# Kernel tuning notes

Hardware: AMD Instinct MI355X
Metric: run time of the kernel (lower is better)

Reference implementation:

```python
import jax, jax.numpy as jnp
import numpy as np

N5, N4, N3, K = 10242, 2562, 642, 7  # icosphere node counts (levels 5,4,3), spatial kernel size
M = 32  # mchannel
EPS = 1e-8


def _sconv(x, neigh, W, b, relu=True):
    # x: [B,T,N,Cin]; neigh: [N,K] 1-ring indices; W: [K,Cin,Cout]
    xn = x[:, :, neigh, :]                        # [B,T,N,K,Cin] irregular gather
    y = jnp.einsum('btnkc,kcd->btnd', xn, W) + b  # per-node kernel contraction
    return jax.nn.relu(y) if relu else y


def _spool(x, pidx):
    # max-pool fine->coarse mesh: pidx [Ncoarse,Kp] indexes fine nodes
    return jnp.max(x[:, :, pidx, :], axis=3)


def _unpool(x, uidx):
    # coarse->fine copy: uidx [Nfine] indexes coarse nodes
    return x[:, :, uidx, :]


def _cos(f, a):
    # torch.nn.CosineSimilarity(dim=-1): dot / max(|f|*|a|, eps)
    dot = jnp.sum(f * a, axis=-1)
    nf = jnp.linalg.norm(f, axis=-1)
    na = jnp.linalg.norm(a, axis=-1)
    return dot / jnp.maximum(nf * na, EPS)


def setup_inputs() -> dict:
    key = jax.random.key(0)
    ks = jax.random.split(key, 32)
    w = lambda i, shape: jax.random.normal(ks[i], shape, jnp.float32) * 0.05
    inp = {
        'frame': jax.random.normal(ks[0], (1, 16, N5, 3), jnp.float32),
        'aem': jax.random.normal(ks[1], (1, 16, N5), jnp.float32),
        'W0f': w(2, (K, 3, M)),        'b0f': w(3, (M,)),
        'W0a': w(4, (K, 1, M)),        'b0a': w(5, (M,)),
        'W1f': w(6, (K, M, 2 * M)),    'b1f': w(7, (2 * M,)),
        'W1a': w(8, (K, M, 2 * M)),    'b1a': w(9, (2 * M,)),
        'W2f': w(10, (K, 2 * M, 4 * M)), 'b2f': w(11, (4 * M,)),
        'W2a': w(12, (K, 2 * M, 4 * M)), 'b2a': w(13, (4 * M,)),
        'W7': w(14, (K, 12 * M, 2 * M)), 'b7': w(15, (2 * M,)),
        'W8': w(16, (K, 4 * M, M)),    'b8': w(17, (M,)),
        'W9': w(18, (K, M, 1)),        'b9': w(19, (1,)),
        'neigh5': jax.random.randint(ks[20], (N5, K), 0, N5),
        'neigh4': jax.random.randint(ks[21], (N4, K), 0, N4),
        'neigh3': jax.random.randint(ks[22], (N3, K), 0, N3),
        'pool5': jax.random.randint(ks[23], (N4, K), 0, N5),
        'pool4': jax.random.randint(ks[24], (N3, K), 0, N4),
        'up4': jax.random.randint(ks[25], (N4,), 0, N3),
        'up5': jax.random.randint(ks[26], (N5,), 0, N4),
        'Tlocation': jax.random.randint(ks[27], (1, 16), 0, 16),
    }
    return inp


def reference(frame, aem, W0f, b0f, W0a, b0a, W1f, b1f, W1a, b1a, W2f, b2f,
              W2a, b2a, W7, b7, W8, b8, W9, b9,
              neigh5, neigh4, neigh3, pool5, pool4, up4, up5, Tlocation):
    a = aem[..., None]                                    # [B,T,N5,1]
    # encoder level 0 (N5)
    c0f = _sconv(frame, neigh5, W0f, b0f)
    c0a = _sconv(a, neigh5, W0a, b0a)
    p0f = _spool(c0f, pool5)
    p0a = _spool(c0a, pool5)
    m0 = _cos(c0f, c0a)[..., None]                        # [B,T,N5,1]
    c0f_att, c0a_att = c0f * m0, c0a * m0
    # encoder level 1 (N4)
    c1f = _sconv(p0f, neigh4, W1f, b1f)
    c1a = _sconv(p0a, neigh4, W1a, b1a)
    p1f = _spool(c1f, pool4)
    p1a = _spool(c1a, pool4)
    m1 = _cos(c1f, c1a)[..., None]
    c1f_att, c1a_att = c1f * m1, c1a * m1
    # bottleneck (N3)
    c2f = _sconv(p1f, neigh3, W2f, b2f)
    c2a = _sconv(p1a, neigh3, W2a, b2a)
    m2 = _cos(c2f, c2a)[..., None]
    conv2 = jnp.concatenate((c2f * m2, c2a * m2), axis=-1)  # [B,T,N3,8M]
    # decoder
    cat7 = jnp.concatenate((_unpool(conv2, up4), c1f_att, c1a_att), axis=-1)  # [B,T,N4,12M]
    conv7 = _sconv(cat7, neigh4, W7, b7)
    cat8 = jnp.concatenate((_unpool(conv7, up5), c0f_att, c0a_att), axis=-1)  # [B,T,N5,4M]
    conv8 = _sconv(cat8, neigh5, W8, b8)
    conv9 = _sconv(conv8, neigh5, W9, b9, relu=False)[..., 0]  # [B,T,N5]
    return jax.nn.softmax(conv9, axis=-1)
```

## Files before the change

kernel.cpp:

```cpp
#include <hip/hip_runtime.h>
#include <cfloat>
#include <cstdint>


constexpr int T  = 16;
constexpr int n5 = 10242, n4 = 2562, n3 = 642;
constexpr int K  = 7;

using bf16x8 = __attribute__((ext_vector_type(8))) short;
using f32x4  = __attribute__((ext_vector_type(4))) float;

static __device__ __forceinline__ float bf2f(unsigned short u) {
    return __uint_as_float((unsigned)u << 16);
}
static __device__ __forceinline__ unsigned short f2bf(float x) {
    unsigned u = __float_as_uint(x);
    u += 0x7FFF + ((u >> 16) & 1);
    return (unsigned short)(u >> 16);
}

__global__ __launch_bounds__(256) void conv0_kernel(
    const float* __restrict__ frame, const float* __restrict__ aem,
    const float* __restrict__ W0f, const float* __restrict__ b0f,
    const float* __restrict__ W0a, const float* __restrict__ b0a,
    const int* __restrict__ neigh5,
    unsigned short* __restrict__ c0f, unsigned short* __restrict__ c0a,
    unsigned short* __restrict__ att0)
{
    const int g = threadIdx.x >> 5;
    const int d = threadIdx.x & 31;
    const int per_t = (n5 + 7) / 8;
    const int t = blockIdx.x / per_t;
    const int n = (blockIdx.x % per_t) * 8 + g;
    if (n >= n5) return;

    float accf = b0f[d];
    float acca = b0a[d];
    const int* nb = neigh5 + n * K;
    #pragma unroll
    for (int k = 0; k < K; ++k) {
        const int j = nb[k];
        const float* fr = frame + ((size_t)t * n5 + j) * 3;
        const float av = aem[(size_t)t * n5 + j];
        accf = fmaf(fr[0], W0f[(k * 3 + 0) * 32 + d], accf);
        accf = fmaf(fr[1], W0f[(k * 3 + 1) * 32 + d], accf);
        accf = fmaf(fr[2], W0f[(k * 3 + 2) * 32 + d], accf);
        acca = fmaf(av, W0a[k * 32 + d], acca);
    }
    accf = fmaxf(accf, 0.f);
    acca = fmaxf(acca, 0.f);

    float dot = accf * acca, ff = accf * accf, aa = acca * acca;
    #pragma unroll
    for (int m = 1; m < 32; m <<= 1) {
        dot += __shfl_xor(dot, m, 32);
        ff  += __shfl_xor(ff,  m, 32);
        aa  += __shfl_xor(aa,  m, 32);
    }
    const float mm = dot / fmaxf(sqrtf(ff) * sqrtf(aa), 1e-8f);
    const size_t base = ((size_t)t * n5 + n) * 32;
    c0f[base + d] = f2bf(accf);
    c0a[base + d] = f2bf(acca);
    const size_t abase = ((size_t)t * n5 + n) * 64;
    att0[abase + d]      = f2bf(accf * mm);
    att0[abase + 32 + d] = f2bf(acca * mm);
}

template<int C>
__global__ __launch_bounds__(256) void pool_kernel(
    const unsigned short* __restrict__ in, const int* __restrict__ pidx,
    int Nin, int Nout, unsigned short* __restrict__ out)
{
    constexpr int C8 = C / 8;
    const int idx = blockIdx.x * 256 + threadIdx.x;
    if (idx >= T * Nout * C8) return;
    const int c8 = idx % C8;
    const int n  = (idx / C8) % Nout;
    const int t  = idx / (C8 * Nout);
    const int* pp = pidx + n * K;
    float m[8];
    #pragma unroll
    for (int j = 0; j < 8; ++j) m[j] = -FLT_MAX;
    #pragma unroll
    for (int k = 0; k < K; ++k) {
        const uint4 v = reinterpret_cast<const uint4*>(in)[((size_t)t * Nin + pp[k]) * C8 + c8];
        const unsigned short* s = reinterpret_cast<const unsigned short*>(&v);
        #pragma unroll
        for (int j = 0; j < 8; ++j) m[j] = fmaxf(m[j], bf2f(s[j]));
    }
    unsigned short o[8];
    #pragma unroll
    for (int j = 0; j < 8; ++j) o[j] = f2bf(m[j]);
    reinterpret_cast<uint4*>(out)[((size_t)t * Nout + n) * C8 + c8] =
        *reinterpret_cast<const uint4*>(o);
}

template<int C, int NN>
__global__ __launch_bounds__(256) void cosatt_kernel(
    const unsigned short* __restrict__ f, const unsigned short* __restrict__ a,
    unsigned short* __restrict__ att)
{
    constexpr int CPL = C / 64;
    const int w = threadIdx.x >> 6, lane = threadIdx.x & 63;
    const int idx = blockIdx.x * 4 + w;
    if (idx >= T * NN) return;
    const unsigned short* fr = f + (size_t)idx * C;
    const unsigned short* ar = a + (size_t)idx * C;
    float xs[CPL], ys[CPL];
    float dot = 0.f, ff = 0.f, aa = 0.f;
    #pragma unroll
    for (int i = 0; i < CPL; ++i) {
        const float x = bf2f(fr[lane + i * 64]);
        const float y = bf2f(ar[lane + i * 64]);
        xs[i] = x; ys[i] = y;
        dot = fmaf(x, y, dot);
        ff  = fmaf(x, x, ff);
        aa  = fmaf(y, y, aa);
    }
    #pragma unroll
    for (int msk = 1; msk < 64; msk <<= 1) {
        dot += __shfl_xor(dot, msk);
        ff  += __shfl_xor(ff,  msk);
        aa  += __shfl_xor(aa,  msk);
    }
    const float m = dot / fmaxf(sqrtf(ff) * sqrtf(aa), 1e-8f);
    unsigned short* orow = att + (size_t)idx * 2 * C;
    #pragma unroll
    for (int i = 0; i < CPL; ++i) {
        orow[lane + i * 64]     = f2bf(xs[i] * m);
        orow[C + lane + i * 64] = f2bf(ys[i] * m);
    }
}

struct PlainB16 {
    const uint4* x; int N; int C8;
    struct Ref { int o; };
    __device__ __forceinline__ Ref prep(int t, int node) const {
        return { (int)(((size_t)t * N + node) * C8) };
    }
    __device__ __forceinline__ uint4 chunk(const Ref& r, int c8) const {
        return x[r.o + c8];
    }
};

struct Cat7B16 {
    const uint4* att2; const uint4* att1; const int* up4;
    struct Ref { int o2, o1; };
    __device__ __forceinline__ Ref prep(int t, int node) const {
        return { (int)(((size_t)t * n3 + up4[node]) * 32),
                 (int)(((size_t)t * n4 + node) * 16) };
    }
    __device__ __forceinline__ uint4 chunk(const Ref& r, int c8) const {
        return (c8 < 32) ? att2[r.o2 + c8] : att1[r.o1 + (c8 - 32)];
    }
};

struct Cat8B16 {
    const uint4* cv7; const uint4* att0; const int* up5;
    struct Ref { int o7, o0; };
    __device__ __forceinline__ Ref prep(int t, int node) const {
        return { (int)(((size_t)t * n4 + up5[node]) * 8),
                 (int)(((size_t)t * n5 + node) * 8) };
    }
    __device__ __forceinline__ uint4 chunk(const Ref& r, int c8) const {
        return (c8 < 8) ? cv7[r.o7 + c8] : att0[r.o0 + (c8 - 8)];
    }
};

__global__ __launch_bounds__(256) void wprep_all_kernel(
    const float* __restrict__ W1f, const float* __restrict__ W1a,
    const float* __restrict__ W2f, const float* __restrict__ W2a,
    const float* __restrict__ W7,  const float* __restrict__ W8,
    unsigned short* __restrict__ Wt1f, unsigned short* __restrict__ Wt1a,
    unsigned short* __restrict__ Wt2f, unsigned short* __restrict__ Wt2a,
    unsigned short* __restrict__ Wt7,  unsigned short* __restrict__ Wt8)
{
    int idx = blockIdx.x * 256 + threadIdx.x;
    const float* W; unsigned short* Wt; int KCv, CO;
    if (idx < 14336)       { W = W1f; Wt = Wt1f; KCv = 224;  CO = 64;  }
    else if (idx < 28672)  { idx -= 14336;  W = W1a; Wt = Wt1a; KCv = 224;  CO = 64;  }
    else if (idx < 86016)  { idx -= 28672;  W = W2f; Wt = Wt2f; KCv = 448;  CO = 128; }
    else if (idx < 143360) { idx -= 86016;  W = W2a; Wt = Wt2a; KCv = 448;  CO = 128; }
    else if (idx < 315392) { idx -= 143360; W = W7;  Wt = Wt7;  KCv = 2688; CO = 64;  }
    else                   { idx -= 315392; W = W8;  Wt = Wt8;  KCv = 896;  CO = 32;  }
    const int d = idx / KCv, kc = idx - d * KCv;
    Wt[idx] = f2bf(W[(size_t)kc * CO + d]);
}

template<int CIN, int COUT, class Loader>
__device__ __forceinline__ void sconv_tile(
    const Loader& ldr, const int* __restrict__ neigh, int N, int t,
    int tile_m, int tile_n,
    const unsigned short* __restrict__ Wt, const float* __restrict__ bias,
    unsigned short* __restrict__ out)
{
    constexpr int KC     = K * CIN;
    constexpr int CHUNKS = CIN / 32;
    constexpr int STEPS  = K * CHUNKS;
    constexpr int D      = STEPS < 3 ? STEPS : 3;

    const int lane = threadIdx.x & 63;
    const int l15 = lane & 15, lhi = lane >> 4;

    const int r0 = tile_m * 32 + l15;
    const int row0 = min(r0, N - 1), row1 = min(r0 + 16, N - 1);

    typename Loader::Ref ref0[K], ref1[K];
    #pragma unroll
    for (int k = 0; k < K; ++k) {
        ref0[k] = ldr.prep(t, neigh[row0 * K + k]);
        ref1[k] = ldr.prep(t, neigh[row1 * K + k]);
    }

    const int col0 = tile_n * 32 + l15;
    const unsigned short* w0p = Wt + (size_t)col0 * KC + lhi * 8;
    const unsigned short* w1p = w0p + (size_t)16 * KC;

    uint4 qa0[D], qa1[D], qb0[D], qb1[D];

    auto issue = [&](int s, int slot) {
        const int k = s / CHUNKS, c = s - k * CHUNKS;
        const int c8 = c * 4 + lhi;
        qa0[slot] = ldr.chunk(ref0[k], c8);
        qa1[slot] = ldr.chunk(ref1[k], c8);
        qb0[slot] = *reinterpret_cast<const uint4*>(w0p + k * CIN + c * 32);
        qb1[slot] = *reinterpret_cast<const uint4*>(w1p + k * CIN + c * 32);
    };

    f32x4 acc[2][2] = {};

    #pragma unroll
    for (int s = 0; s < D; ++s) issue(s, s);
    __builtin_amdgcn_sched_barrier(0);

    #pragma unroll
    for (int s = 0; s < STEPS; ++s) {
        const int slot = s % D;
        const bf16x8 a0 = __builtin_bit_cast(bf16x8, qa0[slot]);
        const bf16x8 a1 = __builtin_bit_cast(bf16x8, qa1[slot]);
        const bf16x8 b0 = __builtin_bit_cast(bf16x8, qb0[slot]);
        const bf16x8 b1 = __builtin_bit_cast(bf16x8, qb1[slot]);
        acc[0][0] = __builtin_amdgcn_mfma_f32_16x16x32_bf16(a0, b0, acc[0][0], 0, 0, 0);
        acc[0][1] = __builtin_amdgcn_mfma_f32_16x16x32_bf16(a0, b1, acc[0][1], 0, 0, 0);
        acc[1][0] = __builtin_amdgcn_mfma_f32_16x16x32_bf16(a1, b0, acc[1][0], 0, 0, 0);
        acc[1][1] = __builtin_amdgcn_mfma_f32_16x16x32_bf16(a1, b1, acc[1][1], 0, 0, 0);
        if (s + D < STEPS) issue(s + D, slot);
        __builtin_amdgcn_sched_barrier(0);
    }

    #pragma unroll
    for (int n = 0; n < 2; ++n) {
        const int gcol = tile_n * 32 + n * 16 + l15;
        const float bv = bias[gcol];
        #pragma unroll
        for (int m = 0; m < 2; ++m) {
            #pragma unroll
            for (int i = 0; i < 4; ++i) {
                const int grow = tile_m * 32 + m * 16 + lhi * 4 + i;
                if (grow < N)
                    out[((size_t)t * N + grow) * COUT + gcol] =
                        f2bf(fmaxf(acc[m][n][i] + bv, 0.f));
            }
        }
    }
}

template<int CIN, int COUT, class Loader>
__global__ __launch_bounds__(64, 2) void sconv_rd_kernel(
    Loader ldr, const int* __restrict__ neigh, int N, int U,
    const unsigned short* __restrict__ Wt, const float* __restrict__ bias,
    unsigned short* __restrict__ out)
{
    constexpr int TN = COUT / 32;
    const int xcd = blockIdx.x & 7;
    int idx = blockIdx.x >> 3;
    const int hi = (idx >= U) ? 1 : 0;
    const int t  = 2 * xcd + hi;
    const int w  = idx - hi * U;
    sconv_tile<CIN, COUT, Loader>(ldr, neigh, N, t, w / TN, w % TN, Wt, bias, out);
}

template<int CIN, int COUT, class Loader>
__global__ __launch_bounds__(64, 2) void sconv_rd2_kernel(
    Loader lf, Loader la, const int* __restrict__ neigh, int N, int U,
    const unsigned short* __restrict__ Wtf, const unsigned short* __restrict__ Wta,
    const float* __restrict__ bf_, const float* __restrict__ ba_,
    unsigned short* __restrict__ of_, unsigned short* __restrict__ oa_)
{
    constexpr int TN = COUT / 32;
    const int xcd = blockIdx.x & 7;
    int idx = blockIdx.x >> 3;
    const int sel = idx & 1; idx >>= 1;
    const int hi = (idx >= U) ? 1 : 0;
    const int t  = 2 * xcd + hi;
    const int w  = idx - hi * U;
    const Loader L = sel ? la : lf;
    const unsigned short* Wt = sel ? Wta : Wtf;
    const float* bias = sel ? ba_ : bf_;
    unsigned short* out = sel ? oa_ : of_;
    sconv_tile<CIN, COUT, Loader>(L, neigh, N, t, w / TN, w % TN, Wt, bias, out);
}

__global__ __launch_bounds__(256) void conv9_kernel(
    const unsigned short* __restrict__ cv8, const int* __restrict__ neigh5,
    const float* __restrict__ W9, const float* __restrict__ b9,
    float* __restrict__ logits)
{
    const int idx = blockIdx.x * 256 + threadIdx.x;
    if (idx >= T * n5) return;
    const int n = idx % n5;
    const int t = idx / n5;
    float acc = b9[0];
    const int* nb = neigh5 + n * K;
    #pragma unroll
    for (int k = 0; k < K; ++k) {
        const uint4* row = reinterpret_cast<const uint4*>(cv8 + ((size_t)t * n5 + nb[k]) * 32);
        const float* wk = W9 + k * 32;
        #pragma unroll
        for (int c4 = 0; c4 < 4; ++c4) {
            const uint4 v = row[c4];
            const unsigned short* s = reinterpret_cast<const unsigned short*>(&v);
            #pragma unroll
            for (int jj = 0; jj < 8; ++jj)
                acc = fmaf(bf2f(s[jj]), wk[c4 * 8 + jj], acc);
        }
    }
    logits[idx] = acc;
}

__global__ __launch_bounds__(1024) void softmax_kernel(
    const float* __restrict__ logits, float* __restrict__ out)
{
    const int t = blockIdx.x, tid = threadIdx.x;
    const float* x = logits + (size_t)t * n5;
    float* y = out + (size_t)t * n5;
    __shared__ float redmax[16], redsum[16];

    float mx = -FLT_MAX;
    for (int i = tid; i < n5; i += 1024) mx = fmaxf(mx, x[i]);
    #pragma unroll
    for (int m = 1; m < 64; m <<= 1) mx = fmaxf(mx, __shfl_xor(mx, m));
    if ((tid & 63) == 0) redmax[tid >> 6] = mx;
    __syncthreads();
    mx = redmax[0];
    #pragma unroll
    for (int i = 1; i < 16; ++i) mx = fmaxf(mx, redmax[i]);

    float s = 0.f;
    for (int i = tid; i < n5; i += 1024) s += expf(x[i] - mx);
    #pragma unroll
    for (int m = 1; m < 64; m <<= 1) s += __shfl_xor(s, m);
    if ((tid & 63) == 0) redsum[tid >> 6] = s;
    __syncthreads();
    s = 0.f;
    #pragma unroll
    for (int i = 0; i < 16; ++i) s += redsum[i];

    for (int i = tid; i < n5; i += 1024) y[i] = expf(x[i] - mx) / s;
}

extern "C" void kernel_launch(void* const* d_in, const int* in_sizes, int n_in,
                              void* d_out, int out_size, void* d_ws, size_t ws_size,
                              hipStream_t stream)
{
    const float* frame = (const float*)d_in[0];
    const float* aem   = (const float*)d_in[1];
    const float* W0f = (const float*)d_in[2];
    const float* b0f = (const float*)d_in[3];
    const float* W0a = (const float*)d_in[4];
    const float* b0a = (const float*)d_in[5];
    const float* W1f = (const float*)d_in[6];
    const float* b1f = (const float*)d_in[7];
    const float* W1a = (const float*)d_in[8];
    const float* b1a = (const float*)d_in[9];
    const float* W2f = (const float*)d_in[10];
    const float* b2f = (const float*)d_in[11];
    const float* W2a = (const float*)d_in[12];
    const float* b2a = (const float*)d_in[13];
    const float* W7  = (const float*)d_in[14];
    const float* b7  = (const float*)d_in[15];
    const float* W8  = (const float*)d_in[16];
    const float* b8  = (const float*)d_in[17];
    const float* W9  = (const float*)d_in[18];
    const float* b9  = (const float*)d_in[19];
    const int* neigh5 = (const int*)d_in[20];
    const int* neigh4 = (const int*)d_in[21];
    const int* neigh3 = (const int*)d_in[22];
    const int* pool5  = (const int*)d_in[23];
    const int* pool4  = (const int*)d_in[24];
    const int* up4    = (const int*)d_in[25];
    const int* up5    = (const int*)d_in[26];

    unsigned short* wsu = (unsigned short*)d_ws;
    size_t off = 0;
    auto ua = [&](size_t n) {
        unsigned short* p = wsu + off; off += (n + 7) & ~(size_t)7; return p;
    };
    unsigned short* c0f  = ua((size_t)T * n5 * 32);
    unsigned short* c0a  = ua((size_t)T * n5 * 32);
    unsigned short* att0 = ua((size_t)T * n5 * 64);
    unsigned short* p0f  = ua((size_t)T * n4 * 32);
    unsigned short* p0a  = ua((size_t)T * n4 * 32);
    unsigned short* c1f  = ua((size_t)T * n4 * 64);
    unsigned short* c1a  = ua((size_t)T * n4 * 64);
    unsigned short* att1 = ua((size_t)T * n4 * 128);
    unsigned short* p1f  = ua((size_t)T * n3 * 64);
    unsigned short* p1a  = ua((size_t)T * n3 * 64);
    unsigned short* c2f  = ua((size_t)T * n3 * 128);
    unsigned short* c2a  = ua((size_t)T * n3 * 128);
    unsigned short* att2 = ua((size_t)T * n3 * 256);
    unsigned short* cv7  = ua((size_t)T * n4 * 64);
    unsigned short* cv8  = ua((size_t)T * n5 * 32);
    unsigned short* Wt1f = ua((size_t)64 * 224);
    unsigned short* Wt1a = ua((size_t)64 * 224);
    unsigned short* Wt2f = ua((size_t)128 * 448);
    unsigned short* Wt2a = ua((size_t)128 * 448);
    unsigned short* Wt7  = ua((size_t)64 * 2688);
    unsigned short* Wt8  = ua((size_t)32 * 896);
    float* lgt = (float*)(wsu + off);

    wprep_all_kernel<<<1344, 256, 0, stream>>>(
        W1f, W1a, W2f, W2a, W7, W8, Wt1f, Wt1a, Wt2f, Wt2a, Wt7, Wt8);

    conv0_kernel<<<T * ((n5 + 7) / 8), 256, 0, stream>>>(
        frame, aem, W0f, b0f, W0a, b0a, neigh5, c0f, c0a, att0);

    {
        const int thr = T * n4 * (32 / 8);
        pool_kernel<32><<<(thr + 255) / 256, 256, 0, stream>>>(c0f, pool5, n5, n4, p0f);
        pool_kernel<32><<<(thr + 255) / 256, 256, 0, stream>>>(c0a, pool5, n5, n4, p0a);
    }

    {
        constexpr int U = 81 * 2;
        sconv_rd2_kernel<32, 64><<<8 * 4 * U, 64, 0, stream>>>(
            PlainB16{(const uint4*)p0f, n4, 4}, PlainB16{(const uint4*)p0a, n4, 4},
            neigh4, n4, U, Wt1f, Wt1a, b1f, b1a, c1f, c1a);
    }
    cosatt_kernel<64, n4><<<(T * n4 + 3) / 4, 256, 0, stream>>>(c1f, c1a, att1);

    {
        const int thr = T * n3 * (64 / 8);
        pool_kernel<64><<<(thr + 255) / 256, 256, 0, stream>>>(c1f, pool4, n4, n3, p1f);
        pool_kernel<64><<<(thr + 255) / 256, 256, 0, stream>>>(c1a, pool4, n4, n3, p1a);
    }

    {
        constexpr int U = 21 * 4;
        sconv_rd2_kernel<64, 128><<<8 * 4 * U, 64, 0, stream>>>(
            PlainB16{(const uint4*)p1f, n3, 8}, PlainB16{(const uint4*)p1a, n3, 8},
            neigh3, n3, U, Wt2f, Wt2a, b2f, b2a, c2f, c2a);
    }
    cosatt_kernel<128, n3><<<(T * n3 + 3) / 4, 256, 0, stream>>>(c2f, c2a, att2);

    {
        constexpr int U = 81 * 2;
        sconv_rd_kernel<384, 64><<<8 * 2 * U, 64, 0, stream>>>(
            Cat7B16{(const uint4*)att2, (const uint4*)att1, up4},
            neigh4, n4, U, Wt7, b7, cv7);
    }

    {
        constexpr int U = 321;
        sconv_rd_kernel<128, 32><<<8 * 2 * U, 64, 0, stream>>>(
            Cat8B16{(const uint4*)cv7, (const uint4*)att0, up5},
            neigh5, n5, U, Wt8, b8, cv8);
    }

    conv9_kernel<<<(T * n5 + 255) / 256, 256, 0, stream>>>(cv8, neigh5, W9, b9, lgt);

    softmax_kernel<<<T, 1024, 0, stream>>>(lgt, (float*)d_out);
}
```

Measured before the change: 330.7 us.

## Restructure decoder convs as dense GEMM then neighbor-gather reduction

For conv7 and conv8, the 7-neighbor gather-then-contract is replaced by a dense per-node GEMM over all K kernel slices, producing Z[node, k*COUT] with no irregular gather on the input side. A separate epilogue kernel then gathers Z rows through the neighbor table, sums the K slices, and adds bias and ReLU. The intent is to turn the gathered-operand MFMA into a regular LDS-tiled GEMM and move the irregular access to a much narrower output tensor. The cost is an extra intermediate buffer written and read as bf16, which adds rounding, plus an additional kernel launch per layer.

```diff
diff --git a/kernel.cpp b/kernel.cpp
--- a/kernel.cpp
+++ b/kernel.cpp
@@ -145,25 +145,19 @@
 
 struct Cat7B16 {
     const uint4* att2; const uint4* att1; const int* up4;
-    struct Ref { int o2, o1; };
-    __device__ __forceinline__ Ref prep(int t, int node) const {
-        return { (int)(((size_t)t * n3 + up4[node]) * 32),
-                 (int)(((size_t)t * n4 + node) * 16) };
-    }
-    __device__ __forceinline__ uint4 chunk(const Ref& r, int c8) const {
-        return (c8 < 32) ? att2[r.o2 + c8] : att1[r.o1 + (c8 - 32)];
+    __device__ __forceinline__ uint4 row8(int t, int node, int c8) const {
+        if (c8 < 32)
+            return att2[((size_t)t * n3 + up4[node]) * 32 + c8];
+        return att1[((size_t)t * n4 + node) * 16 + (c8 - 32)];
     }
 };
 
 struct Cat8B16 {
     const uint4* cv7; const uint4* att0; const int* up5;
-    struct Ref { int o7, o0; };
-    __device__ __forceinline__ Ref prep(int t, int node) const {
-        return { (int)(((size_t)t * n4 + up5[node]) * 8),
-                 (int)(((size_t)t * n5 + node) * 8) };
-    }
-    __device__ __forceinline__ uint4 chunk(const Ref& r, int c8) const {
-        return (c8 < 8) ? cv7[r.o7 + c8] : att0[r.o0 + (c8 - 8)];
+    __device__ __forceinline__ uint4 row8(int t, int node, int c8) const {
+        if (c8 < 8)
+            return cv7[((size_t)t * n4 + up5[node]) * 8 + c8];
+        return att0[((size_t)t * n5 + node) * 8 + (c8 - 8)];
     }
 };
 
@@ -185,6 +179,144 @@
     else                   { idx -= 315392; W = W8;  Wt = Wt8;  KCv = 896;  CO = 32;  }
     const int d = idx / KCv, kc = idx - d * KCv;
     Wt[idx] = f2bf(W[(size_t)kc * CO + d]);
+}
+
+template<int CIN, int COUT, int BM, int BN, class Loader>
+__global__ __launch_bounds__(256) void gemm_z_kernel(
+    Loader ldr, int N, int Mt,
+    const unsigned short* __restrict__ Wt,
+    unsigned short* __restrict__ Z)
+{
+    constexpr int KC   = K * CIN;
+    constexpr int ND   = K * COUT;
+    constexpr int BK   = 64;
+    constexpr int KSTEPS = CIN / BK;
+    constexpr int U4R  = BK / 8;
+    constexpr int WGR_N = BN / 32;
+    constexpr int WGR_M = 4 / WGR_N;
+    constexpr int DG   = COUT / BN;
+    constexpr int NT   = K * DG;
+    constexpr int VPTA = BM * U4R / 256;
+    constexpr int VPTW = BN * U4R / 256 > 0 ? BN * U4R / 256 : 1;
+    static_assert(BM == WGR_M * 32 && CIN % BK == 0 && BN * U4R >= 256);
+
+    __shared__ __align__(16) unsigned short As[BM * BK];
+    __shared__ __align__(16) unsigned short Ws[BN * BK];
+
+    const int xcd = blockIdx.x & 7;
+    int rest = blockIdx.x >> 3;
+    const int half = Mt * NT;
+    const int hi = (rest >= half) ? 1 : 0;
+    const int t  = 2 * xcd + hi;
+    const int j  = rest - hi * half;
+    const int tile_m = j / NT;
+    const int tnk    = j % NT;
+    const int kk_ = tnk / DG;
+    const int dg  = tnk % DG;
+
+    const int tid = threadIdx.x, lane = tid & 63, wave = tid >> 6;
+    const int wr = wave / WGR_N, wc = wave % WGR_N;
+    const int l15 = lane & 15, lhi = lane >> 4;
+    const int m0 = tile_m * BM;
+
+    f32x4 acc[2][2] = {};
+
+    for (int ks = 0; ks < KSTEPS; ++ks) {
+        uint4 av[VPTA];
+        #pragma unroll
+        for (int v = 0; v < VPTA; ++v) {
+            const int g = tid + v * 256, row = g / U4R, c8 = g % U4R;
+            av[v] = ldr.row8(t, min(m0 + row, N - 1), ks * U4R + c8);
+        }
+        uint4 wv[VPTW];
+        #pragma unroll
+        for (int v = 0; v < VPTW; ++v) {
+            const int g = tid + v * 256, d = g / U4R, c8 = g % U4R;
+            wv[v] = *reinterpret_cast<const uint4*>(
+                Wt + (size_t)(dg * BN + d) * KC + kk_ * CIN + ks * BK + c8 * 8);
+        }
+
+        __syncthreads();
+        #pragma unroll
+        for (int v = 0; v < VPTA; ++v) {
+            const int g = tid + v * 256, row = g / U4R, c8 = g % U4R;
+            *reinterpret_cast<uint4*>(&As[(row * BK + c8 * 8) ^ ((row & 7) << 3)]) = av[v];
+        }
+        #pragma unroll
+        for (int v = 0; v < VPTW; ++v) {
+            const int g = tid + v * 256, d = g / U4R, c8 = g % U4R;
+            *reinterpret_cast<uint4*>(&Ws[(d * BK + c8 * 8) ^ ((d & 7) << 3)]) = wv[v];
+        }
+        __syncthreads();
+
+        #pragma unroll
+        for (int kk2 = 0; kk2 < BK / 32; ++kk2) {
+            const int kb = kk2 * 32 + lhi * 8;
+            bf16x8 a[2], b[2];
+            #pragma unroll
+            for (int m = 0; m < 2; ++m) {
+                const int row = wr * 32 + m * 16 + l15;
+                a[m] = *reinterpret_cast<const bf16x8*>(&As[(row * BK + kb) ^ ((row & 7) << 3)]);
+            }
+            #pragma unroll
+            for (int n = 0; n < 2; ++n) {
+                const int col = wc * 32 + n * 16 + l15;
+                b[n] = *reinterpret_cast<const bf16x8*>(&Ws[(col * BK + kb) ^ ((col & 7) << 3)]);
+            }
+            #pragma unroll
+            for (int m = 0; m < 2; ++m)
+                #pragma unroll
+                for (int n = 0; n < 2; ++n)
+                    acc[m][n] = __builtin_amdgcn_mfma_f32_16x16x32_bf16(a[m], b[n], acc[m][n], 0, 0, 0);
+        }
+    }
+
+    const int zc0 = kk_ * COUT + dg * BN;
+    #pragma unroll
+    for (int n = 0; n < 2; ++n) {
+        const int gcol = zc0 + wc * 32 + n * 16 + l15;
+        #pragma unroll
+        for (int m = 0; m < 2; ++m) {
+            #pragma unroll
+            for (int i = 0; i < 4; ++i) {
+                const int grow = m0 + wr * 32 + m * 16 + lhi * 4 + i;
+                if (grow < N)
+                    Z[((size_t)t * N + grow) * ND + gcol] = f2bf(acc[m][n][i]);
+            }
+        }
+    }
+}
+
+template<int COUT>
+__global__ __launch_bounds__(256) void epi_reduce_kernel(
+    const unsigned short* __restrict__ Z, const int* __restrict__ neigh, int N,
+    const float* __restrict__ bias, unsigned short* __restrict__ out)
+{
+    constexpr int ND = K * COUT;
+    constexpr int C8 = COUT / 8;
+    const int idx = blockIdx.x * 256 + threadIdx.x;
+    if (idx >= T * N * C8) return;
+    const int c8 = idx % C8;
+    const int n  = (idx / C8) % N;
+    const int t  = idx / (C8 * N);
+    const int* nb = neigh + n * K;
+
+    float s[8];
+    #pragma unroll
+    for (int j = 0; j < 8; ++j) s[j] = bias[c8 * 8 + j];
+    #pragma unroll
+    for (int k = 0; k < K; ++k) {
+        const uint4 v = *reinterpret_cast<const uint4*>(
+            &Z[((size_t)t * N + nb[k]) * ND + k * COUT + c8 * 8]);
+        const unsigned short* p = reinterpret_cast<const unsigned short*>(&v);
+        #pragma unroll
+        for (int j = 0; j < 8; ++j) s[j] += bf2f(p[j]);
+    }
+    unsigned short o[8];
+    #pragma unroll
+    for (int j = 0; j < 8; ++j) o[j] = f2bf(fmaxf(s[j], 0.f));
+    *reinterpret_cast<uint4*>(&out[((size_t)t * N + n) * COUT + c8 * 8]) =
+        *reinterpret_cast<const uint4*>(o);
 }
 
 template<int CIN, int COUT, class Loader>
@@ -263,21 +395,6 @@
             }
         }
     }
-}
-
-template<int CIN, int COUT, class Loader>
-__global__ __launch_bounds__(64, 2) void sconv_rd_kernel(
-    Loader ldr, const int* __restrict__ neigh, int N, int U,
-    const unsigned short* __restrict__ Wt, const float* __restrict__ bias,
-    unsigned short* __restrict__ out)
-{
-    constexpr int TN = COUT / 32;
-    const int xcd = blockIdx.x & 7;
-    int idx = blockIdx.x >> 3;
-    const int hi = (idx >= U) ? 1 : 0;
-    const int t  = 2 * xcd + hi;
-    const int w  = idx - hi * U;
-    sconv_tile<CIN, COUT, Loader>(ldr, neigh, N, t, w / TN, w % TN, Wt, bias, out);
 }
 
 template<int CIN, int COUT, class Loader>
@@ -417,7 +534,8 @@
     unsigned short* Wt2a = ua((size_t)128 * 448);
     unsigned short* Wt7  = ua((size_t)64 * 2688);
     unsigned short* Wt8  = ua((size_t)32 * 896);
-    float* lgt = (float*)(wsu + off);
+    unsigned short* Zbuf = ua((size_t)T * n5 * 224);
+    float* lgt = (float*)(wsu + ((off + 1) & ~(size_t)1));
 
     wprep_all_kernel<<<1344, 256, 0, stream>>>(
         W1f, W1a, W2f, W2a, W7, W8, Wt1f, Wt1a, Wt2f, Wt2a, Wt7, Wt8);
@@ -454,17 +572,21 @@
     cosatt_kernel<128, n3><<<(T * n3 + 3) / 4, 256, 0, stream>>>(c2f, c2a, att2);
 
     {
-        constexpr int U = 81 * 2;
-        sconv_rd_kernel<384, 64><<<8 * 2 * U, 64, 0, stream>>>(
-            Cat7B16{(const uint4*)att2, (const uint4*)att1, up4},
-            neigh4, n4, U, Wt7, b7, cv7);
+        constexpr int Mt = (n4 + 63) / 64;
+        gemm_z_kernel<384, 64, 64, 64><<<16 * Mt * 7, 256, 0, stream>>>(
+            Cat7B16{(const uint4*)att2, (const uint4*)att1, up4}, n4, Mt, Wt7, Zbuf);
+        const int thr = T * n4 * 8;
+        epi_reduce_kernel<64><<<(thr + 255) / 256, 256, 0, stream>>>(
+            Zbuf, neigh4, n4, b7, cv7);
     }
 
     {
-        constexpr int U = 321;
-        sconv_rd_kernel<128, 32><<<8 * 2 * U, 64, 0, stream>>>(
-            Cat8B16{(const uint4*)cv7, (const uint4*)att0, up5},
-            neigh5, n5, U, Wt8, b8, cv8);
+        constexpr int Mt = (n5 + 127) / 128;
+        gemm_z_kernel<128, 32, 128, 32><<<16 * Mt * 7, 256, 0, stream>>>(
+            Cat8B16{(const uint4*)cv7, (const uint4*)att0, up5}, n5, Mt, Wt8, Zbuf);
+        const int thr = T * n5 * 4;
+        epi_reduce_kernel<32><<<(thr + 255) / 256, 256, 0, stream>>>(
+            Zbuf, neigh5, n5, b8, cv8);
     }
 
     conv9_kernel<<<(T * n5 + 255) / 256, 256, 0, stream>>>(cv8, neigh5, W9, b9, lgt);
```

Result: faster. 279.1 us (-15.6%).
